# Performance work log

Measured on AMD Instinct MI355X. Metric: run time of the kernel, lower is better.

## Reference

```python
import jax, jax.numpy as jnp
import numpy as np

B, N, F_IN, F_OUT = 8, 2048, 128, 128


def setup_inputs() -> dict:
    key = jax.random.key(0)
    k1, k2, k3, k4 = jax.random.split(key, 4)
    h = jax.random.normal(k1, (B, N, F_IN), dtype=jnp.float32)
    adj = (jax.random.uniform(k2, (B, N, N)) > 0.5).astype(jnp.float32)
    adj = jnp.maximum(adj, jnp.eye(N, dtype=jnp.float32)[None])
    # torch nn.Linear weights: W is [out_features, in_features], a is [1, 2*out_features]
    W = jax.random.normal(k3, (F_OUT, F_IN), dtype=jnp.float32) * 0.05
    a = jax.random.normal(k4, (1, 2 * F_OUT), dtype=jnp.float32) * 0.05
    return {"h": h, "adj": adj, "W": W, "a": a}


def reference(h, adj, W, a):
    # Wh = W(h): [B, N, F_OUT]
    Wh = jnp.einsum("bnf,of->bno", h, W)
    # attn_fc(concat(Wh_i, Wh_j)) == (Wh_i @ a1) + (Wh_j @ a2): exact split of the
    # linear layer, avoiding the O(B*N*N*2F) concat intermediate.
    a1 = a[0, :F_OUT]
    a2 = a[0, F_OUT:]
    e_i = Wh @ a1  # [B, N]  score contribution of destination node i
    e_j = Wh @ a2  # [B, N]  score contribution of source node j
    e = e_i[:, :, None] + e_j[:, None, :]  # [B, N, N]
    e = e + (1.0 - adj) * (-1e9)
    alpha = jax.nn.softmax(e, axis=-1)  # [B, N, N]
    # weighted aggregation: h_out[b,i] = sum_j alpha[b,i,j] * Wh[b,j]
    h_out = jnp.einsum("bij,bjo->bio", alpha, Wh)
    return h_out
```

## Files before the change

### kernel.cpp

```cpp
#include <hip/hip_runtime.h>
#include <stdint.h>

#define AS1 __attribute__((address_space(1)))
#define AS3 __attribute__((address_space(3)))

typedef __bf16 bf16x8 __attribute__((ext_vector_type(8)));
typedef float f32x4 __attribute__((ext_vector_type(4)));

constexpr int NB = 8;
constexpr int N  = 2048;
constexpr int F  = 128;

__device__ __forceinline__ unsigned short bf16r(float f) {
    unsigned u = __float_as_uint(f);
    return (unsigned short)((u + 0x7FFFu + ((u >> 16) & 1u)) >> 16);
}
__device__ __forceinline__ float bf2f(unsigned short s) {
    return __uint_as_float(((unsigned)s) << 16);
}


__global__ __launch_bounds__(256) void k1_wh(const float* __restrict__ h,
                                             const float* __restrict__ W,
                                             const float* __restrict__ a,
                                             unsigned short* __restrict__ Wb2,
                                             unsigned short* __restrict__ p16) {
    __shared__ float epart[2][64];

    const int tid  = threadIdx.x;
    const int lane = tid & 63, wid = tid >> 6;
    const int quad = lane >> 4, l15 = lane & 15;
    const int wm = wid >> 1, wn = wid & 1;
    const int m0 = blockIdx.x * 64;
    const int batch = m0 >> 11;
    const int nbase = m0 & 2047;

    f32x4 acc[2][4] = {};

#pragma unroll
    for (int kk = 0; kk < 4; ++kk) {
        const int k = kk * 32 + quad * 8;
        bf16x8 afr[2], bfr[4];
#pragma unroll
        for (int rt = 0; rt < 2; ++rt) {
            const float* src = h + (size_t)(m0 + wm * 32 + rt * 16 + l15) * F + k;
            float4 x0 = *(const float4*)src;
            float4 x1 = *(const float4*)(src + 4);
            afr[rt][0] = (__bf16)x0.x; afr[rt][1] = (__bf16)x0.y;
            afr[rt][2] = (__bf16)x0.z; afr[rt][3] = (__bf16)x0.w;
            afr[rt][4] = (__bf16)x1.x; afr[rt][5] = (__bf16)x1.y;
            afr[rt][6] = (__bf16)x1.z; afr[rt][7] = (__bf16)x1.w;
        }
#pragma unroll
        for (int ct = 0; ct < 4; ++ct) {
            const int o = wn * 64 + ct * 16 + l15;
            const float* src = W + (size_t)o * F + k;
            float4 x0 = *(const float4*)src;
            float4 x1 = *(const float4*)(src + 4);
            bfr[ct][0] = (__bf16)x0.x; bfr[ct][1] = (__bf16)x0.y;
            bfr[ct][2] = (__bf16)x0.z; bfr[ct][3] = (__bf16)x0.w;
            bfr[ct][4] = (__bf16)x1.x; bfr[ct][5] = (__bf16)x1.y;
            bfr[ct][6] = (__bf16)x1.z; bfr[ct][7] = (__bf16)x1.w;
        }
#pragma unroll
        for (int rt = 0; rt < 2; ++rt)
#pragma unroll
            for (int ct = 0; ct < 4; ++ct)
                acc[rt][ct] = __builtin_amdgcn_mfma_f32_16x16x32_bf16(
                    afr[rt], bfr[ct], acc[rt][ct], 0, 0, 0);
    }

    float a2v[4];
#pragma unroll
    for (int ct = 0; ct < 4; ++ct) a2v[ct] = a[F + wn * 64 + ct * 16 + l15];

    float ep[2][4];
#pragma unroll
    for (int rt = 0; rt < 2; ++rt)
#pragma unroll
        for (int g = 0; g < 4; ++g) {
            float s = 0.f;
#pragma unroll
            for (int ct = 0; ct < 4; ++ct) s += acc[rt][ct][g] * a2v[ct];
            ep[rt][g] = s;
        }
#pragma unroll
    for (int m = 1; m < 16; m <<= 1)
#pragma unroll
        for (int rt = 0; rt < 2; ++rt)
#pragma unroll
            for (int g = 0; g < 4; ++g)
                ep[rt][g] += __shfl_xor(ep[rt][g], m);

    if (l15 == 0)
#pragma unroll
        for (int rt = 0; rt < 2; ++rt)
#pragma unroll
            for (int g = 0; g < 4; ++g)
                epart[wn][wm * 32 + rt * 16 + quad * 4 + g] = ep[rt][g];
    __syncthreads();

#pragma unroll
    for (int rt = 0; rt < 2; ++rt)
#pragma unroll
        for (int ct = 0; ct < 4; ++ct) {
            const int o  = wn * 64 + ct * 16 + l15;
            const int r0 = wm * 32 + rt * 16 + quad * 4;
            const int n0 = nbase + r0;
            ushort4 v;
#pragma unroll
            for (int g = 0; g < 4; ++g) {
                const float e  = epart[0][r0 + g] + epart[1][r0 + g];
                const float pf = bf2f(bf16r(expf(e)));
                (&v.x)[g] = bf16r(pf * acc[rt][ct][g]);
            }
            size_t off = (size_t)batch * N * F + (size_t)(n0 >> 3) * 1024 + o * 8 + (n0 & 7);
            *(ushort4*)&Wb2[off] = v;
        }

    if (tid < 64) {
        const float e = epart[0][tid] + epart[1][tid];
        p16[batch * N + nbase + tid] = bf16r(expf(e));
    }
}

__global__ __launch_bounds__(256, 2) void k3_fused(const float* __restrict__ adj,
                                                   const unsigned short* __restrict__ Wb2,
                                                   const unsigned short* __restrict__ p16,
                                                   float* __restrict__ out) {
    __shared__ __align__(16) char Asm_[3][8192];
    __shared__ __align__(16) char Bsm_[3][16384];
    __shared__ __align__(16) char Psm_[4096];

    const int tid  = threadIdx.x;
    const int lane = tid & 63, wid = tid >> 6;
    const int quad = lane >> 4, l15 = lane & 15;
    const int wm = wid >> 1, wn = wid & 1;
    const int b  = blockIdx.x & 7;
    const int it = blockIdx.x >> 3;
    const int i0 = it * 32;
    const int rowL = wm * 16 + l15;

    const float* aSrc[2];
#pragma unroll
    for (int s = 0; s < 2; ++s) {
        const int rl = (wid * 2 + s) * 4 + (lane >> 4);
        const int G  = (lane & 15) ^ (rl & 15);
        aSrc[s] = adj + (size_t)b * N * N + (size_t)(i0 + rl) * N + G * 4;
    }
    const char* bSrc = (const char*)Wb2 + (size_t)b * (N * F * 2)
                     + wid * 4096 + lane * 16;
    const char* pSrc = (const char*)p16 + (size_t)b * N * 2 + lane * 16;

#define K3_STAGE(BI, C)                                                            \
    do {                                                                           \
        __builtin_amdgcn_global_load_lds((const AS1 void*)(aSrc[0] + (C) * 64),    \
            (AS3 void*)(&Asm_[BI][(wid * 2 + 0) * 1024]), 16, 0, 0);               \
        __builtin_amdgcn_global_load_lds((const AS1 void*)(aSrc[1] + (C) * 64),    \
            (AS3 void*)(&Asm_[BI][(wid * 2 + 1) * 1024]), 16, 0, 0);               \
        __builtin_amdgcn_global_load_lds(                                          \
            (const AS1 void*)(bSrc + (size_t)(C) * 16384 + 0 * 1024),              \
            (AS3 void*)(&Bsm_[BI][wid * 4096 + 0 * 1024]), 16, 0, 0);              \
        __builtin_amdgcn_global_load_lds(                                          \
            (const AS1 void*)(bSrc + (size_t)(C) * 16384 + 1 * 1024),              \
            (AS3 void*)(&Bsm_[BI][wid * 4096 + 1 * 1024]), 16, 0, 0);              \
        __builtin_amdgcn_global_load_lds(                                          \
            (const AS1 void*)(bSrc + (size_t)(C) * 16384 + 2 * 1024),              \
            (AS3 void*)(&Bsm_[BI][wid * 4096 + 2 * 1024]), 16, 0, 0);              \
        __builtin_amdgcn_global_load_lds(                                          \
            (const AS1 void*)(bSrc + (size_t)(C) * 16384 + 3 * 1024),              \
            (AS3 void*)(&Bsm_[BI][wid * 4096 + 3 * 1024]), 16, 0, 0);              \
    } while (0)

    f32x4 acc0 = {}, acc1 = {}, acc2 = {}, acc3 = {};
    f32x4 dacc = {0.f, 0.f, 0.f, 0.f};

    if (wid == 0) {
#pragma unroll
        for (int s = 0; s < 4; ++s)
            __builtin_amdgcn_global_load_lds((const AS1 void*)(pSrc + s * 1024),
                (AS3 void*)(&Psm_[s * 1024]), 16, 0, 0);
    }
    K3_STAGE(0, 0);
    K3_STAGE(1, 1);
    K3_STAGE(2, 2);

#define K3_CHUNK(C, BI, WAITSTR, DOSTAGE)                                          \
    {                                                                              \
        asm volatile(WAITSTR ::: "memory");                                        \
        __builtin_amdgcn_s_barrier();                                              \
        __builtin_amdgcn_sched_barrier(0);                                         \
        const char* aB = &Asm_[BI][0];                                             \
        const char* bB = &Bsm_[BI][0];                                             \
        _Pragma("unroll")                                                          \
        for (int ks = 0; ks < 2; ++ks) {                                           \
            f32x4 x0 = *(const f32x4*)(aB + rowL * 256                             \
                          + (((ks * 8 + quad * 2 + 0) ^ l15) << 4));               \
            f32x4 x1 = *(const f32x4*)(aB + rowL * 256                             \
                          + (((ks * 8 + quad * 2 + 1) ^ l15) << 4));               \
            bf16x8 af;                                                             \
            af[0] = (__bf16)x0[0]; af[1] = (__bf16)x0[1];                          \
            af[2] = (__bf16)x0[2]; af[3] = (__bf16)x0[3];                          \
            af[4] = (__bf16)x1[0]; af[5] = (__bf16)x1[1];                          \
            af[6] = (__bf16)x1[2]; af[7] = (__bf16)x1[3];                          \
            bf16x8 pv = *(const bf16x8*)(&Psm_[(C) * 128 + ks * 64 + quad * 16]);  \
            bf16x8 bf0 = *(const bf16x8*)(bB + ks * 8192 + quad * 2048             \
                                          + wn * 1024 + 0 * 256 + l15 * 16);       \
            bf16x8 bf1 = *(const bf16x8*)(bB + ks * 8192 + quad * 2048             \
                                          + wn * 1024 + 1 * 256 + l15 * 16);       \
            bf16x8 bf2 = *(const bf16x8*)(bB + ks * 8192 + quad * 2048             \
                                          + wn * 1024 + 2 * 256 + l15 * 16);       \
            bf16x8 bf3 = *(const bf16x8*)(bB + ks * 8192 + quad * 2048             \
                                          + wn * 1024 + 3 * 256 + l15 * 16);       \
            acc0 = __builtin_amdgcn_mfma_f32_16x16x32_bf16(af, bf0, acc0, 0, 0, 0);\
            acc1 = __builtin_amdgcn_mfma_f32_16x16x32_bf16(af, bf1, acc1, 0, 0, 0);\
            acc2 = __builtin_amdgcn_mfma_f32_16x16x32_bf16(af, bf2, acc2, 0, 0, 0);\
            acc3 = __builtin_amdgcn_mfma_f32_16x16x32_bf16(af, bf3, acc3, 0, 0, 0);\
            dacc = __builtin_amdgcn_mfma_f32_16x16x32_bf16(af, pv,  dacc, 0, 0, 0);\
        }                                                                          \
        if (DOSTAGE) {                                                             \
            __builtin_amdgcn_s_barrier();                                          \
            __builtin_amdgcn_sched_barrier(0);                                     \
            K3_STAGE(BI, (C) + 3);                                                 \
        }                                                                          \
    }

    for (int c3 = 0; c3 < 27; c3 += 3) {
        K3_CHUNK(c3 + 0, 0, "s_waitcnt vmcnt(12)", 1)
        K3_CHUNK(c3 + 1, 1, "s_waitcnt vmcnt(12)", 1)
        K3_CHUNK(c3 + 2, 2, "s_waitcnt vmcnt(12)", 1)
    }
    K3_CHUNK(27, 0, "s_waitcnt vmcnt(12)", 1)
    K3_CHUNK(28, 1, "s_waitcnt vmcnt(12)", 1)
    K3_CHUNK(29, 2, "s_waitcnt vmcnt(12)", 0)
    K3_CHUNK(30, 0, "s_waitcnt vmcnt(6)",  0)
    K3_CHUNK(31, 1, "s_waitcnt vmcnt(0)",  0)

#undef K3_CHUNK
#undef K3_STAGE

#pragma unroll
    for (int g = 0; g < 4; ++g) {
        const float inv = 1.0f / dacc[g];
        float* orow = out + ((size_t)b * N + i0 + wm * 16 + quad * 4 + g) * F
                    + wn * 64 + l15;
        orow[0]  = acc0[g] * inv;
        orow[16] = acc1[g] * inv;
        orow[32] = acc2[g] * inv;
        orow[48] = acc3[g] * inv;
    }
}

extern "C" void kernel_launch(void* const* d_in, const int* in_sizes, int n_in,
                              void* d_out, int out_size, void* d_ws, size_t ws_size,
                              hipStream_t stream) {
    const float* h   = (const float*)d_in[0];
    const float* adj = (const float*)d_in[1];
    const float* W   = (const float*)d_in[2];
    const float* a   = (const float*)d_in[3];
    float* out = (float*)d_out;

    unsigned short* Wb2 = (unsigned short*)d_ws;
    unsigned short* p16 = (unsigned short*)((char*)d_ws + (4u << 20));

    k1_wh<<<NB * N / 64, 256, 0, stream>>>(h, W, a, Wb2, p16);
    k3_fused<<<NB * 64, 256, 0, stream>>>(adj, Wb2, p16, out);
}
```

Measured before the change: 221.7 us.

## Shrink k3 row tile to 16 and double-buffer to raise block count and occupancy

```diff
diff --git a/kernel.cpp b/kernel.cpp
--- a/kernel.cpp
+++ b/kernel.cpp
@@ -124,29 +124,26 @@
     }
 }
 
-__global__ __launch_bounds__(256, 2) void k3_fused(const float* __restrict__ adj,
+__global__ __launch_bounds__(256, 3) void k3_fused(const float* __restrict__ adj,
                                                    const unsigned short* __restrict__ Wb2,
                                                    const unsigned short* __restrict__ p16,
                                                    float* __restrict__ out) {
-    __shared__ __align__(16) char Asm_[3][8192];
-    __shared__ __align__(16) char Bsm_[3][16384];
+    __shared__ __align__(16) char Asm_[2][4096];
+    __shared__ __align__(16) char Bsm_[2][16384];
     __shared__ __align__(16) char Psm_[4096];
 
     const int tid  = threadIdx.x;
     const int lane = tid & 63, wid = tid >> 6;
     const int quad = lane >> 4, l15 = lane & 15;
-    const int wm = wid >> 1, wn = wid & 1;
     const int b  = blockIdx.x & 7;
     const int it = blockIdx.x >> 3;
-    const int i0 = it * 32;
-    const int rowL = wm * 16 + l15;
-
-    const float* aSrc[2];
-#pragma unroll
-    for (int s = 0; s < 2; ++s) {
-        const int rl = (wid * 2 + s) * 4 + (lane >> 4);
-        const int G  = (lane & 15) ^ (rl & 15);
-        aSrc[s] = adj + (size_t)b * N * N + (size_t)(i0 + rl) * N + G * 4;
+    const int i0 = it * 16;
+
+    const float* aSrc;
+    {
+        const int rl = wid * 4 + (lane >> 4);
+        const int G  = (lane & 15) ^ rl;
+        aSrc = adj + (size_t)b * N * N + (size_t)(i0 + rl) * N + G * 4;
     }
     const char* bSrc = (const char*)Wb2 + (size_t)b * (N * F * 2)
                      + wid * 4096 + lane * 16;
@@ -154,10 +151,8 @@
 
 #define K3_STAGE(BI, C)                                                            \
     do {                                                                           \
-        __builtin_amdgcn_global_load_lds((const AS1 void*)(aSrc[0] + (C) * 64),    \
-            (AS3 void*)(&Asm_[BI][(wid * 2 + 0) * 1024]), 16, 0, 0);               \
-        __builtin_amdgcn_global_load_lds((const AS1 void*)(aSrc[1] + (C) * 64),    \
-            (AS3 void*)(&Asm_[BI][(wid * 2 + 1) * 1024]), 16, 0, 0);               \
+        __builtin_amdgcn_global_load_lds((const AS1 void*)(aSrc + (C) * 64),       \
+            (AS3 void*)(&Asm_[BI][wid * 1024]), 16, 0, 0);                         \
         __builtin_amdgcn_global_load_lds(                                          \
             (const AS1 void*)(bSrc + (size_t)(C) * 16384 + 0 * 1024),              \
             (AS3 void*)(&Bsm_[BI][wid * 4096 + 0 * 1024]), 16, 0, 0);              \
@@ -172,7 +167,7 @@
             (AS3 void*)(&Bsm_[BI][wid * 4096 + 3 * 1024]), 16, 0, 0);              \
     } while (0)
 
-    f32x4 acc0 = {}, acc1 = {}, acc2 = {}, acc3 = {};
+    f32x4 acc0 = {}, acc1 = {};
     f32x4 dacc = {0.f, 0.f, 0.f, 0.f};
 
     if (wid == 0) {
@@ -183,7 +178,6 @@
     }
     K3_STAGE(0, 0);
     K3_STAGE(1, 1);
-    K3_STAGE(2, 2);
 
 #define K3_CHUNK(C, BI, WAITSTR, DOSTAGE)                                          \
     {                                                                              \
@@ -194,47 +188,36 @@
         const char* bB = &Bsm_[BI][0];                                             \
         _Pragma("unroll")                                                          \
         for (int ks = 0; ks < 2; ++ks) {                                           \
-            f32x4 x0 = *(const f32x4*)(aB + rowL * 256                             \
-                          + (((ks * 8 + quad * 2 + 0) ^ l15) << 4));               \
-            f32x4 x1 = *(const f32x4*)(aB + rowL * 256                             \
-                          + (((ks * 8 + quad * 2 + 1) ^ l15) << 4));               \
+            const int G0 = ks * 8 + quad * 2;                                      \
+            f32x4 x0 = *(const f32x4*)(aB + l15 * 256 + (((G0 + 0) ^ l15) << 4));  \
+            f32x4 x1 = *(const f32x4*)(aB + l15 * 256 + (((G0 + 1) ^ l15) << 4));  \
             bf16x8 af;                                                             \
             af[0] = (__bf16)x0[0]; af[1] = (__bf16)x0[1];                          \
             af[2] = (__bf16)x0[2]; af[3] = (__bf16)x0[3];                          \
             af[4] = (__bf16)x1[0]; af[5] = (__bf16)x1[1];                          \
             af[6] = (__bf16)x1[2]; af[7] = (__bf16)x1[3];                          \
             bf16x8 pv = *(const bf16x8*)(&Psm_[(C) * 128 + ks * 64 + quad * 16]);  \
-            bf16x8 bf0 = *(const bf16x8*)(bB + ks * 8192 + quad * 2048             \
-                                          + wn * 1024 + 0 * 256 + l15 * 16);       \
-            bf16x8 bf1 = *(const bf16x8*)(bB + ks * 8192 + quad * 2048             \
-                                          + wn * 1024 + 1 * 256 + l15 * 16);       \
-            bf16x8 bf2 = *(const bf16x8*)(bB + ks * 8192 + quad * 2048             \
-                                          + wn * 1024 + 2 * 256 + l15 * 16);       \
-            bf16x8 bf3 = *(const bf16x8*)(bB + ks * 8192 + quad * 2048             \
-                                          + wn * 1024 + 3 * 256 + l15 * 16);       \
+            bf16x8 bf0 = *(const bf16x8*)(bB + (ks * 4 + quad) * 2048              \
+                                          + (wid * 32 + 0)  * 16 + l15 * 16);      \
+            bf16x8 bf1 = *(const bf16x8*)(bB + (ks * 4 + quad) * 2048              \
+                                          + (wid * 32 + 16) * 16 + l15 * 16);      \
             acc0 = __builtin_amdgcn_mfma_f32_16x16x32_bf16(af, bf0, acc0, 0, 0, 0);\
             acc1 = __builtin_amdgcn_mfma_f32_16x16x32_bf16(af, bf1, acc1, 0, 0, 0);\
-            acc2 = __builtin_amdgcn_mfma_f32_16x16x32_bf16(af, bf2, acc2, 0, 0, 0);\
-            acc3 = __builtin_amdgcn_mfma_f32_16x16x32_bf16(af, bf3, acc3, 0, 0, 0);\
             dacc = __builtin_amdgcn_mfma_f32_16x16x32_bf16(af, pv,  dacc, 0, 0, 0);\
         }                                                                          \
         if (DOSTAGE) {                                                             \
             __builtin_amdgcn_s_barrier();                                          \
             __builtin_amdgcn_sched_barrier(0);                                     \
-            K3_STAGE(BI, (C) + 3);                                                 \
+            K3_STAGE(BI, (C) + 2);                                                 \
         }                                                                          \
     }
 
-    for (int c3 = 0; c3 < 27; c3 += 3) {
-        K3_CHUNK(c3 + 0, 0, "s_waitcnt vmcnt(12)", 1)
-        K3_CHUNK(c3 + 1, 1, "s_waitcnt vmcnt(12)", 1)
-        K3_CHUNK(c3 + 2, 2, "s_waitcnt vmcnt(12)", 1)
-    }
-    K3_CHUNK(27, 0, "s_waitcnt vmcnt(12)", 1)
-    K3_CHUNK(28, 1, "s_waitcnt vmcnt(12)", 1)
-    K3_CHUNK(29, 2, "s_waitcnt vmcnt(12)", 0)
-    K3_CHUNK(30, 0, "s_waitcnt vmcnt(6)",  0)
-    K3_CHUNK(31, 1, "s_waitcnt vmcnt(0)",  0)
+    for (int c2 = 0; c2 < 30; c2 += 2) {
+        K3_CHUNK(c2 + 0, 0, "s_waitcnt vmcnt(5)", 1)
+        K3_CHUNK(c2 + 1, 1, "s_waitcnt vmcnt(5)", 1)
+    }
+    K3_CHUNK(30, 0, "s_waitcnt vmcnt(5)", 0)
+    K3_CHUNK(31, 1, "s_waitcnt vmcnt(0)", 0)
 
 #undef K3_CHUNK
 #undef K3_STAGE
@@ -242,12 +225,10 @@
 #pragma unroll
     for (int g = 0; g < 4; ++g) {
         const float inv = 1.0f / dacc[g];
-        float* orow = out + ((size_t)b * N + i0 + wm * 16 + quad * 4 + g) * F
-                    + wn * 64 + l15;
+        float* orow = out + ((size_t)b * N + i0 + quad * 4 + g) * F
+                    + wid * 32 + l15;
         orow[0]  = acc0[g] * inv;
         orow[16] = acc1[g] * inv;
-        orow[32] = acc2[g] * inv;
-        orow[48] = acc3[g] * inv;
     }
 }
 
@@ -264,5 +245,5 @@
     unsigned short* p16 = (unsigned short*)((char*)d_ws + (4u << 20));
 
     k1_wh<<<NB * N / 64, 256, 0, stream>>>(h, W, a, Wb2, p16);
-    k3_fused<<<NB * 64, 256, 0, stream>>>(adj, Wb2, p16, out);
-}
+    k3_fused<<<NB * 128, 256, 0, stream>>>(adj, Wb2, p16, out);
+}
```

Result: slower. 251.1 us (+13.3%).

## Enlarge k3 tile to 64 rows with 8 waves sharing each Wh chunk

Applied to the files above, without the earlier changes.

```diff
diff --git a/kernel.cpp b/kernel.cpp
--- a/kernel.cpp
+++ b/kernel.cpp
@@ -124,22 +124,21 @@
     }
 }
 
-__global__ __launch_bounds__(256, 2) void k3_fused(const float* __restrict__ adj,
+__global__ __launch_bounds__(512, 2) void k3_fused(const float* __restrict__ adj,
                                                    const unsigned short* __restrict__ Wb2,
                                                    const unsigned short* __restrict__ p16,
                                                    float* __restrict__ out) {
-    __shared__ __align__(16) char Asm_[3][8192];
+    __shared__ __align__(16) char Asm_[3][16384];
     __shared__ __align__(16) char Bsm_[3][16384];
     __shared__ __align__(16) char Psm_[4096];
 
     const int tid  = threadIdx.x;
     const int lane = tid & 63, wid = tid >> 6;
     const int quad = lane >> 4, l15 = lane & 15;
-    const int wm = wid >> 1, wn = wid & 1;
+    const int wr = wid >> 2, wc = wid & 3;
     const int b  = blockIdx.x & 7;
     const int it = blockIdx.x >> 3;
-    const int i0 = it * 32;
-    const int rowL = wm * 16 + l15;
+    const int i0 = it * 64;
 
     const float* aSrc[2];
 #pragma unroll
@@ -149,7 +148,7 @@
         aSrc[s] = adj + (size_t)b * N * N + (size_t)(i0 + rl) * N + G * 4;
     }
     const char* bSrc = (const char*)Wb2 + (size_t)b * (N * F * 2)
-                     + wid * 4096 + lane * 16;
+                     + wid * 2048 + lane * 16;
     const char* pSrc = (const char*)p16 + (size_t)b * N * 2 + lane * 16;
 
 #define K3_STAGE(BI, C)                                                            \
@@ -160,20 +159,14 @@
             (AS3 void*)(&Asm_[BI][(wid * 2 + 1) * 1024]), 16, 0, 0);               \
         __builtin_amdgcn_global_load_lds(                                          \
             (const AS1 void*)(bSrc + (size_t)(C) * 16384 + 0 * 1024),              \
-            (AS3 void*)(&Bsm_[BI][wid * 4096 + 0 * 1024]), 16, 0, 0);              \
+            (AS3 void*)(&Bsm_[BI][wid * 2048 + 0 * 1024]), 16, 0, 0);              \
         __builtin_amdgcn_global_load_lds(                                          \
             (const AS1 void*)(bSrc + (size_t)(C) * 16384 + 1 * 1024),              \
-            (AS3 void*)(&Bsm_[BI][wid * 4096 + 1 * 1024]), 16, 0, 0);              \
-        __builtin_amdgcn_global_load_lds(                                          \
-            (const AS1 void*)(bSrc + (size_t)(C) * 16384 + 2 * 1024),              \
-            (AS3 void*)(&Bsm_[BI][wid * 4096 + 2 * 1024]), 16, 0, 0);              \
-        __builtin_amdgcn_global_load_lds(                                          \
-            (const AS1 void*)(bSrc + (size_t)(C) * 16384 + 3 * 1024),              \
-            (AS3 void*)(&Bsm_[BI][wid * 4096 + 3 * 1024]), 16, 0, 0);              \
+            (AS3 void*)(&Bsm_[BI][wid * 2048 + 1 * 1024]), 16, 0, 0);              \
     } while (0)
 
-    f32x4 acc0 = {}, acc1 = {}, acc2 = {}, acc3 = {};
-    f32x4 dacc = {0.f, 0.f, 0.f, 0.f};
+    f32x4 acc[2][2] = {};
+    f32x4 dacc[2] = {};
 
     if (wid == 0) {
 #pragma unroll
@@ -194,29 +187,34 @@
         const char* bB = &Bsm_[BI][0];                                             \
         _Pragma("unroll")                                                          \
         for (int ks = 0; ks < 2; ++ks) {                                           \
-            f32x4 x0 = *(const f32x4*)(aB + rowL * 256                             \
-                          + (((ks * 8 + quad * 2 + 0) ^ l15) << 4));               \
-            f32x4 x1 = *(const f32x4*)(aB + rowL * 256                             \
-                          + (((ks * 8 + quad * 2 + 1) ^ l15) << 4));               \
-            bf16x8 af;                                                             \
-            af[0] = (__bf16)x0[0]; af[1] = (__bf16)x0[1];                          \
-            af[2] = (__bf16)x0[2]; af[3] = (__bf16)x0[3];                          \
-            af[4] = (__bf16)x1[0]; af[5] = (__bf16)x1[1];                          \
-            af[6] = (__bf16)x1[2]; af[7] = (__bf16)x1[3];                          \
             bf16x8 pv = *(const bf16x8*)(&Psm_[(C) * 128 + ks * 64 + quad * 16]);  \
-            bf16x8 bf0 = *(const bf16x8*)(bB + ks * 8192 + quad * 2048             \
-                                          + wn * 1024 + 0 * 256 + l15 * 16);       \
-            bf16x8 bf1 = *(const bf16x8*)(bB + ks * 8192 + quad * 2048             \
-                                          + wn * 1024 + 1 * 256 + l15 * 16);       \
-            bf16x8 bf2 = *(const bf16x8*)(bB + ks * 8192 + quad * 2048             \
-                                          + wn * 1024 + 2 * 256 + l15 * 16);       \
-            bf16x8 bf3 = *(const bf16x8*)(bB + ks * 8192 + quad * 2048             \
-                                          + wn * 1024 + 3 * 256 + l15 * 16);       \
-            acc0 = __builtin_amdgcn_mfma_f32_16x16x32_bf16(af, bf0, acc0, 0, 0, 0);\
-            acc1 = __builtin_amdgcn_mfma_f32_16x16x32_bf16(af, bf1, acc1, 0, 0, 0);\
-            acc2 = __builtin_amdgcn_mfma_f32_16x16x32_bf16(af, bf2, acc2, 0, 0, 0);\
-            acc3 = __builtin_amdgcn_mfma_f32_16x16x32_bf16(af, bf3, acc3, 0, 0, 0);\
-            dacc = __builtin_amdgcn_mfma_f32_16x16x32_bf16(af, pv,  dacc, 0, 0, 0);\
+            bf16x8 af[2];                                                          \
+            _Pragma("unroll")                                                      \
+            for (int rt = 0; rt < 2; ++rt) {                                       \
+                const int row = wr * 32 + rt * 16 + l15;                           \
+                const int G0  = ks * 8 + quad * 2;                                 \
+                f32x4 x0 = *(const f32x4*)(aB + row * 256                          \
+                              + (((G0 + 0) ^ (row & 15)) << 4));                   \
+                f32x4 x1 = *(const f32x4*)(aB + row * 256                          \
+                              + (((G0 + 1) ^ (row & 15)) << 4));                   \
+                af[rt][0] = (__bf16)x0[0]; af[rt][1] = (__bf16)x0[1];              \
+                af[rt][2] = (__bf16)x0[2]; af[rt][3] = (__bf16)x0[3];              \
+                af[rt][4] = (__bf16)x1[0]; af[rt][5] = (__bf16)x1[1];              \
+                af[rt][6] = (__bf16)x1[2]; af[rt][7] = (__bf16)x1[3];              \
+            }                                                                      \
+            _Pragma("unroll")                                                      \
+            for (int ct = 0; ct < 2; ++ct) {                                       \
+                bf16x8 bf = *(const bf16x8*)(bB + (ks * 4 + quad) * 2048           \
+                                + (wc * 32 + ct * 16) * 16 + l15 * 16);            \
+                acc[0][ct] = __builtin_amdgcn_mfma_f32_16x16x32_bf16(              \
+                    af[0], bf, acc[0][ct], 0, 0, 0);                               \
+                acc[1][ct] = __builtin_amdgcn_mfma_f32_16x16x32_bf16(              \
+                    af[1], bf, acc[1][ct], 0, 0, 0);                               \
+            }                                                                      \
+            dacc[0] = __builtin_amdgcn_mfma_f32_16x16x32_bf16(                     \
+                af[0], pv, dacc[0], 0, 0, 0);                                      \
+            dacc[1] = __builtin_amdgcn_mfma_f32_16x16x32_bf16(                     \
+                af[1], pv, dacc[1], 0, 0, 0);                                      \
         }                                                                          \
         if (DOSTAGE) {                                                             \
             __builtin_amdgcn_s_barrier();                                          \
@@ -226,29 +224,29 @@
     }
 
     for (int c3 = 0; c3 < 27; c3 += 3) {
-        K3_CHUNK(c3 + 0, 0, "s_waitcnt vmcnt(12)", 1)
-        K3_CHUNK(c3 + 1, 1, "s_waitcnt vmcnt(12)", 1)
-        K3_CHUNK(c3 + 2, 2, "s_waitcnt vmcnt(12)", 1)
-    }
-    K3_CHUNK(27, 0, "s_waitcnt vmcnt(12)", 1)
-    K3_CHUNK(28, 1, "s_waitcnt vmcnt(12)", 1)
-    K3_CHUNK(29, 2, "s_waitcnt vmcnt(12)", 0)
-    K3_CHUNK(30, 0, "s_waitcnt vmcnt(6)",  0)
-    K3_CHUNK(31, 1, "s_waitcnt vmcnt(0)",  0)
+        K3_CHUNK(c3 + 0, 0, "s_waitcnt vmcnt(8)", 1)
+        K3_CHUNK(c3 + 1, 1, "s_waitcnt vmcnt(8)", 1)
+        K3_CHUNK(c3 + 2, 2, "s_waitcnt vmcnt(8)", 1)
+    }
+    K3_CHUNK(27, 0, "s_waitcnt vmcnt(8)", 1)
+    K3_CHUNK(28, 1, "s_waitcnt vmcnt(8)", 1)
+    K3_CHUNK(29, 2, "s_waitcnt vmcnt(8)", 0)
+    K3_CHUNK(30, 0, "s_waitcnt vmcnt(4)", 0)
+    K3_CHUNK(31, 1, "s_waitcnt vmcnt(0)", 0)
 
 #undef K3_CHUNK
 #undef K3_STAGE
 
 #pragma unroll
-    for (int g = 0; g < 4; ++g) {
-        const float inv = 1.0f / dacc[g];
-        float* orow = out + ((size_t)b * N + i0 + wm * 16 + quad * 4 + g) * F
-                    + wn * 64 + l15;
-        orow[0]  = acc0[g] * inv;
-        orow[16] = acc1[g] * inv;
-        orow[32] = acc2[g] * inv;
-        orow[48] = acc3[g] * inv;
-    }
+    for (int rt = 0; rt < 2; ++rt)
+#pragma unroll
+        for (int g = 0; g < 4; ++g) {
+            const float inv = 1.0f / dacc[rt][g];
+            float* orow = out + ((size_t)b * N + i0 + wr * 32 + rt * 16
+                                 + quad * 4 + g) * F + wc * 32 + l15;
+            orow[0]  = acc[rt][0][g] * inv;
+            orow[16] = acc[rt][1][g] * inv;
+        }
 }
 
 extern "C" void kernel_launch(void* const* d_in, const int* in_sizes, int n_in,
@@ -264,5 +262,5 @@
     unsigned short* p16 = (unsigned short*)((char*)d_ws + (4u << 20));
 
     k1_wh<<<NB * N / 64, 256, 0, stream>>>(h, W, a, Wb2, p16);
-    k3_fused<<<NB * 64, 256, 0, stream>>>(adj, Wb2, p16, out);
-}
+    k3_fused<<<NB * 32, 512, 0, stream>>>(adj, Wb2, p16, out);
+}
```

New measurement: 217.5 us. About the same (-1.9%).
